# Optimization experiments

Measured on AMD Instinct MI355X. Metric: run time of the kernel, lower is better.

Reference implementation:

```python
import jax, jax.numpy as jnp
import numpy as np

NTOKENS = 6144
SPLIT = 2048          # splits = [0, 2048, inf]
TEMP = 65.0
N, D = 128, 256


def setup_inputs() -> dict:
    key = jax.random.key(0)
    k1, k2, k3, k4, k5, k6 = jax.random.split(key, 6)
    hiddens = jax.random.normal(k1, (N, D), dtype=jnp.float32)
    targets = jax.random.randint(k2, (N,), 0, NTOKENS)
    emb = jax.random.normal(k3, (NTOKENS + 1, D), dtype=jnp.float32)  # +1 tail-target token
    W = jax.random.normal(k4, (D, D), dtype=jnp.float32) / np.sqrt(D)
    U = jax.random.normal(k5, (D, D), dtype=jnp.float32) / np.sqrt(D)
    b = jax.random.normal(k6, (D,), dtype=jnp.float32)
    return {"hiddens": hiddens, "targets": targets, "emb": emb, "W": W, "U": U, "b": b}


def _logprob(h, words_emb, W, U, b):
    # h: [N, d]; words_emb: [V, d]
    # surrogate one-step RNN-cell model: out = tanh(E[w] @ W + h @ U + b) -> [N, V, d]
    out = jnp.tanh(words_emb @ W + (h @ U + b)[:, None, :])
    # SimpleEuclDistance: squared euclidean distance per (hidden, word)
    dist = jnp.sum((h[:, None, :] - out) ** 2, axis=-1)          # [N, V]
    # SimplePolynomialKernel: k(d) = 1 / (1 + d), scaled by temp
    k = TEMP / (1.0 + dist)
    return jax.nn.log_softmax(k, axis=-1)


def reference(hiddens, targets, emb, W, U, b):
    n_head = SPLIT            # head words 0..SPLIT-1
    n_tail = NTOKENS - SPLIT  # tail words SPLIT..NTOKENS-1
    # head vocab = head words + the single tail-target token (index NTOKENS)
    head_ids = jnp.concatenate([jnp.arange(n_head), jnp.array([NTOKENS])])
    lp_head = _logprob(hiddens, emb[head_ids], W, U, b)          # [N, n_head+1]
    lp_tail = _logprob(hiddens, emb[SPLIT:NTOKENS], W, U, b)     # [N, n_tail]

    is_head = targets < SPLIT
    head_idx = jnp.clip(targets, 0, n_head - 1)
    tail_idx = jnp.clip(targets - SPLIT, 0, n_tail - 1)
    head_loss = -jnp.take_along_axis(lp_head, head_idx[:, None], axis=1)[:, 0]
    # for tail tokens: head part is the tail-target column (last col, softmaxed_head_res[:, -1])
    tail_loss = -(lp_head[:, -1] + jnp.take_along_axis(lp_tail, tail_idx[:, None], axis=1)[:, 0])
    per_token = jnp.where(is_head, head_loss, tail_loss)
    return jnp.sum(per_token) / targets.shape[0]
```

## Files before the change

### kernel.cpp

```cpp
#include <hip/hip_runtime.h>
#include <hip/hip_bf16.h>
#include <cfloat>

#define V_ALL  6145
#define SPLIT_ 2048
#define NROW   128
#define DDIM   256
#define TEMP_  65.0f
#define KS     6160

#define EW_OFF 0
#define EW_SZ  (V_ALL * DDIM)
#define HU_OFF (EW_OFF + EW_SZ)
#define HU_SZ  (NROW * DDIM)
#define RL_OFF (HU_OFF + HU_SZ)
#define RL_SZ  NROW
#define K_OFF  ((RL_OFF + RL_SZ + 3) & ~3)

__global__ __launch_bounds__(256) void k_hu(const float* __restrict__ h,
                                            const float* __restrict__ U,
                                            const float* __restrict__ b,
                                            float* __restrict__ hU) {
    const int d = threadIdx.x;
    const int n = blockIdx.x;
    const float4* __restrict__ hr = (const float4*)(h + n * DDIM);
    float acc = b[d];
    #pragma unroll 8
    for (int k4 = 0; k4 < DDIM / 4; ++k4) {
        float4 hv = hr[k4];
        int k = k4 * 4;
        acc = fmaf(hv.x, U[(k + 0) * DDIM + d], acc);
        acc = fmaf(hv.y, U[(k + 1) * DDIM + d], acc);
        acc = fmaf(hv.z, U[(k + 2) * DDIM + d], acc);
        acc = fmaf(hv.w, U[(k + 3) * DDIM + d], acc);
    }
    hU[n * DDIM + d] = acc;
}

__global__ __launch_bounds__(256) void k_ew(const float* __restrict__ emb,
                                            const float* __restrict__ W,
                                            float* __restrict__ EW) {
    const int d = threadIdx.x;
    const int v0 = blockIdx.x * 8;
    const float4* __restrict__ er[8];
    #pragma unroll
    for (int i = 0; i < 8; ++i) {
        int r = v0 + i;
        if (r > V_ALL - 1) r = V_ALL - 1;
        er[i] = (const float4*)(emb + r * DDIM);
    }
    float acc[8];
    #pragma unroll
    for (int i = 0; i < 8; ++i) acc[i] = 0.f;

    for (int k4 = 0; k4 < DDIM / 4; ++k4) {
        const int k = k4 * 4;
        const float w0 = W[(k + 0) * DDIM + d];
        const float w1 = W[(k + 1) * DDIM + d];
        const float w2 = W[(k + 2) * DDIM + d];
        const float w3 = W[(k + 3) * DDIM + d];
        #pragma unroll
        for (int i = 0; i < 8; ++i) {
            float4 e = er[i][k4];
            acc[i] = fmaf(e.x, w0, acc[i]);
            acc[i] = fmaf(e.y, w1, acc[i]);
            acc[i] = fmaf(e.z, w2, acc[i]);
            acc[i] = fmaf(e.w, w3, acc[i]);
        }
    }
    #pragma unroll
    for (int i = 0; i < 8; ++i) {
        int r = v0 + i;
        if (r <= V_ALL - 1) EW[r * DDIM + d] = acc[i];
    }
}

__device__ __forceinline__ float tanh_fast(float x) {
    float ex = __expf(2.f * x);
    return fmaf(-2.f, __builtin_amdgcn_rcpf(ex + 1.f), 1.f);
}

__global__ __launch_bounds__(256) void k_dist(const float* __restrict__ EW,
                                              const float* __restrict__ hU,
                                              const float* __restrict__ h,
                                              float* __restrict__ Km) {
    __shared__ float sEW[16][260];
    __shared__ float sHU[16][260];
    __shared__ float sH [16][260];

    const int v0 = blockIdx.x * 16;
    const int n0 = blockIdx.y * 16;

    #pragma unroll
    for (int j = 0; j < 4; ++j) {
        int idx = threadIdx.x + 256 * j;
        int r   = idx >> 6;
        int c4  = idx & 63;
        int vr  = v0 + r; if (vr > V_ALL - 1) vr = V_ALL - 1;
        *(float4*)&sEW[r][c4 * 4] = *(const float4*)&EW[vr * DDIM + c4 * 4];
        *(float4*)&sHU[r][c4 * 4] = *(const float4*)&hU[(n0 + r) * DDIM + c4 * 4];
        *(float4*)&sH [r][c4 * 4] = *(const float4*)&h [(n0 + r) * DDIM + c4 * 4];
    }
    __syncthreads();

    const int vl = threadIdx.x & 15;
    const int nl = threadIdx.x >> 4;
    const float* pe = &sEW[vl][0];
    const float* pa = &sHU[nl][0];
    const float* ph = &sH [nl][0];

    float acc = 0.f;
    #pragma unroll 4
    for (int d4 = 0; d4 < DDIM / 4; ++d4) {
        float4 e  = *(const float4*)(pe + d4 * 4);
        float4 a  = *(const float4*)(pa + d4 * 4);
        float4 hh = *(const float4*)(ph + d4 * 4);
        { float t = tanh_fast(e.x + a.x); float df = hh.x - t; acc = fmaf(df, df, acc); }
        { float t = tanh_fast(e.y + a.y); float df = hh.y - t; acc = fmaf(df, df, acc); }
        { float t = tanh_fast(e.z + a.z); float df = hh.z - t; acc = fmaf(df, df, acc); }
        { float t = tanh_fast(e.w + a.w); float df = hh.w - t; acc = fmaf(df, df, acc); }
    }
    float kk = TEMP_ / (1.f + acc);
    int vg = v0 + vl;
    if (vg <= V_ALL - 1) Km[(n0 + nl) * KS + vg] = kk;
}

__device__ __forceinline__ float block_max(float x, volatile float* s4) {
    #pragma unroll
    for (int o = 32; o; o >>= 1) x = fmaxf(x, __shfl_down(x, o));
    __syncthreads();
    if ((threadIdx.x & 63) == 0) s4[threadIdx.x >> 6] = x;
    __syncthreads();
    return fmaxf(fmaxf(s4[0], s4[1]), fmaxf(s4[2], s4[3]));
}
__device__ __forceinline__ float block_sum(float x, volatile float* s4) {
    #pragma unroll
    for (int o = 32; o; o >>= 1) x += __shfl_down(x, o);
    __syncthreads();
    if ((threadIdx.x & 63) == 0) s4[threadIdx.x >> 6] = x;
    __syncthreads();
    return s4[0] + s4[1] + s4[2] + s4[3];
}

__global__ __launch_bounds__(256) void k_lse(const float* __restrict__ Km,
                                             const int* __restrict__ targets,
                                             float* __restrict__ rowloss) {
    __shared__ float s4[4];
    const int n = blockIdx.x;
    const int tid = threadIdx.x;
    const float* row = Km + n * KS;

    float m = -FLT_MAX;
    for (int v = tid; v < SPLIT_ + 1; v += 256) {
        int c = (v == SPLIT_) ? (V_ALL - 1) : v;
        m = fmaxf(m, row[c]);
    }
    float hmax = block_max(m, s4);
    float s = 0.f;
    for (int v = tid; v < SPLIT_ + 1; v += 256) {
        int c = (v == SPLIT_) ? (V_ALL - 1) : v;
        s += __expf(row[c] - hmax);
    }
    float hsum = block_sum(s, s4);

    m = -FLT_MAX;
    for (int v = tid; v < 4096; v += 256) m = fmaxf(m, row[SPLIT_ + v]);
    float tmax = block_max(m, s4);
    s = 0.f;
    for (int v = tid; v < 4096; v += 256) s += __expf(row[SPLIT_ + v] - tmax);
    float tsum = block_sum(s, s4);

    if (tid == 0) {
        float logZh = hmax + logf(hsum);
        float logZt = tmax + logf(tsum);
        int t = targets[n];
        float loss;
        if (t < SPLIT_) loss = logZh - row[t];
        else            loss = logZh + logZt - row[V_ALL - 1] - row[t];
        rowloss[n] = loss;
    }
}

__global__ __launch_bounds__(128) void k_final(const float* __restrict__ rowloss,
                                               float* __restrict__ out) {
    const int tid = threadIdx.x;
    float x = rowloss[tid];
    #pragma unroll
    for (int o = 32; o; o >>= 1) x += __shfl_down(x, o);
    __shared__ float s[2];
    if ((tid & 63) == 0) s[tid >> 6] = x;
    __syncthreads();
    if (tid == 0) out[0] = (s[0] + s[1]) / (float)NROW;
}

extern "C" void kernel_launch(void* const* d_in, const int* in_sizes, int n_in,
                              void* d_out, int out_size, void* d_ws, size_t ws_size,
                              hipStream_t stream) {
    const float* h       = (const float*)d_in[0];
    const int*   targets = (const int*)  d_in[1];
    const float* emb     = (const float*)d_in[2];
    const float* W       = (const float*)d_in[3];
    const float* U       = (const float*)d_in[4];
    const float* b       = (const float*)d_in[5];

    float* ws = (float*)d_ws;
    float* EW = ws + EW_OFF;
    float* hU = ws + HU_OFF;
    float* rl = ws + RL_OFF;
    float* Km = ws + K_OFF;

    k_hu  <<<dim3(NROW),      dim3(256), 0, stream>>>(h, U, b, hU);
    k_ew  <<<dim3(769),       dim3(256), 0, stream>>>(emb, W, EW);
    k_dist<<<dim3(385, 8),    dim3(256), 0, stream>>>(EW, hU, h, Km);
    k_lse <<<dim3(NROW),      dim3(256), 0, stream>>>(Km, targets, rl);
    k_final<<<dim3(1),        dim3(128), 0, stream>>>(rl, (float*)d_out);
}
```

Baseline: 188.4 us.

## Fuse softmax sums into distance kernel using fixed max and atomics

The distance kernel now computes exp(k-65) directly, using the known upper bound of k (TEMP), and reduces those values over 16-lane groups. It atomically adds the sums into per-row head and tail accumulators and records the target and tail-token kernel values. This removes the full K matrix write, the separate log-sum-exp kernel and a launch. The tanh scaling by 2/ln2 is folded into the EW and hU precomputation so exp2 can be used directly. In exchange it adds atomic contention and a nondeterministic summation order.

Result: faster. 181.5 us (-3.6%).

```diff
diff --git a/kernel.cpp b/kernel.cpp
--- a/kernel.cpp
+++ b/kernel.cpp
@@ -3,26 +3,32 @@
 #include <cfloat>
 
 #define V_ALL  6145
+#define NTOK   6144
 #define SPLIT_ 2048
 #define NROW   128
 #define DDIM   256
 #define TEMP_  65.0f
-#define KS     6160
+#define C2     2.8853900817779268f
 
 #define EW_OFF 0
 #define EW_SZ  (V_ALL * DDIM)
 #define HU_OFF (EW_OFF + EW_SZ)
 #define HU_SZ  (NROW * DDIM)
-#define RL_OFF (HU_OFF + HU_SZ)
-#define RL_SZ  NROW
-#define K_OFF  ((RL_OFF + RL_SZ + 3) & ~3)
+#define HS_OFF (HU_OFF + HU_SZ)
+#define TS_OFF (HS_OFF + NROW)
+#define KT_OFF (TS_OFF + NROW)
+#define KL_OFF (KT_OFF + NROW)
 
 __global__ __launch_bounds__(256) void k_hu(const float* __restrict__ h,
                                             const float* __restrict__ U,
                                             const float* __restrict__ b,
-                                            float* __restrict__ hU) {
+                                            float* __restrict__ hUs,
+                                            float* __restrict__ hsum,
+                                            float* __restrict__ tsum) {
     const int d = threadIdx.x;
     const int n = blockIdx.x;
+    if (d == 0) hsum[n] = 0.f;
+    if (d == 1) tsum[n] = 0.f;
     const float4* __restrict__ hr = (const float4*)(h + n * DDIM);
     float acc = b[d];
     #pragma unroll 8
@@ -34,12 +40,12 @@
         acc = fmaf(hv.z, U[(k + 2) * DDIM + d], acc);
         acc = fmaf(hv.w, U[(k + 3) * DDIM + d], acc);
     }
-    hU[n * DDIM + d] = acc;
+    hUs[n * DDIM + d] = C2 * acc;
 }
 
 __global__ __launch_bounds__(256) void k_ew(const float* __restrict__ emb,
                                             const float* __restrict__ W,
-                                            float* __restrict__ EW) {
+                                            float* __restrict__ EWs) {
     const int d = threadIdx.x;
     const int v0 = blockIdx.x * 8;
     const float4* __restrict__ er[8];
@@ -71,19 +77,18 @@
     #pragma unroll
     for (int i = 0; i < 8; ++i) {
         int r = v0 + i;
-        if (r <= V_ALL - 1) EW[r * DDIM + d] = acc[i];
-    }
-}
-
-__device__ __forceinline__ float tanh_fast(float x) {
-    float ex = __expf(2.f * x);
-    return fmaf(-2.f, __builtin_amdgcn_rcpf(ex + 1.f), 1.f);
-}
-
-__global__ __launch_bounds__(256) void k_dist(const float* __restrict__ EW,
-                                              const float* __restrict__ hU,
+        if (r <= V_ALL - 1) EWs[r * DDIM + d] = C2 * acc[i];
+    }
+}
+
+__global__ __launch_bounds__(256) void k_dist(const float* __restrict__ EWs,
+                                              const float* __restrict__ hUs,
                                               const float* __restrict__ h,
-                                              float* __restrict__ Km) {
+                                              const int* __restrict__ targets,
+                                              float* __restrict__ hsum,
+                                              float* __restrict__ tsum,
+                                              float* __restrict__ ktarget,
+                                              float* __restrict__ ktail) {
     __shared__ float sEW[16][260];
     __shared__ float sHU[16][260];
     __shared__ float sH [16][260];
@@ -97,9 +102,9 @@
         int r   = idx >> 6;
         int c4  = idx & 63;
         int vr  = v0 + r; if (vr > V_ALL - 1) vr = V_ALL - 1;
-        *(float4*)&sEW[r][c4 * 4] = *(const float4*)&EW[vr * DDIM + c4 * 4];
-        *(float4*)&sHU[r][c4 * 4] = *(const float4*)&hU[(n0 + r) * DDIM + c4 * 4];
-        *(float4*)&sH [r][c4 * 4] = *(const float4*)&h [(n0 + r) * DDIM + c4 * 4];
+        *(float4*)&sEW[r][c4 * 4] = *(const float4*)&EWs[vr * DDIM + c4 * 4];
+        *(float4*)&sHU[r][c4 * 4] = *(const float4*)&hUs[(n0 + r) * DDIM + c4 * 4];
+        *(float4*)&sH [r][c4 * 4] = *(const float4*)&h  [(n0 + r) * DDIM + c4 * 4];
     }
     __syncthreads();
 
@@ -109,88 +114,68 @@
     const float* pa = &sHU[nl][0];
     const float* ph = &sH [nl][0];
 
-    float acc = 0.f;
+    float acc0 = 0.f, acc1 = 0.f;
     #pragma unroll 4
     for (int d4 = 0; d4 < DDIM / 4; ++d4) {
         float4 e  = *(const float4*)(pe + d4 * 4);
         float4 a  = *(const float4*)(pa + d4 * 4);
         float4 hh = *(const float4*)(ph + d4 * 4);
-        { float t = tanh_fast(e.x + a.x); float df = hh.x - t; acc = fmaf(df, df, acc); }
-        { float t = tanh_fast(e.y + a.y); float df = hh.y - t; acc = fmaf(df, df, acc); }
-        { float t = tanh_fast(e.z + a.z); float df = hh.z - t; acc = fmaf(df, df, acc); }
-        { float t = tanh_fast(e.w + a.w); float df = hh.w - t; acc = fmaf(df, df, acc); }
-    }
-    float kk = TEMP_ / (1.f + acc);
-    int vg = v0 + vl;
-    if (vg <= V_ALL - 1) Km[(n0 + nl) * KS + vg] = kk;
-}
-
-__device__ __forceinline__ float block_max(float x, volatile float* s4) {
-    #pragma unroll
-    for (int o = 32; o; o >>= 1) x = fmaxf(x, __shfl_down(x, o));
+        { float ex = __builtin_amdgcn_exp2f(e.x + a.x);
+          float t  = fmaf(-2.f, __builtin_amdgcn_rcpf(ex + 1.f), 1.f);
+          float df = hh.x - t; acc0 = fmaf(df, df, acc0); }
+        { float ex = __builtin_amdgcn_exp2f(e.y + a.y);
+          float t  = fmaf(-2.f, __builtin_amdgcn_rcpf(ex + 1.f), 1.f);
+          float df = hh.y - t; acc1 = fmaf(df, df, acc1); }
+        { float ex = __builtin_amdgcn_exp2f(e.z + a.z);
+          float t  = fmaf(-2.f, __builtin_amdgcn_rcpf(ex + 1.f), 1.f);
+          float df = hh.z - t; acc0 = fmaf(df, df, acc0); }
+        { float ex = __builtin_amdgcn_exp2f(e.w + a.w);
+          float t  = fmaf(-2.f, __builtin_amdgcn_rcpf(ex + 1.f), 1.f);
+          float df = hh.w - t; acc1 = fmaf(df, df, acc1); }
+    }
+    const float kk = TEMP_ / (1.f + acc0 + acc1);
+
+    const int vg = v0 + vl;
+    const int n  = n0 + nl;
+    const bool valid = (vg <= NTOK);
+    float ek = valid ? __expf(kk - 65.f) : 0.f;
+
+    ek += __shfl_xor(ek, 1, 16);
+    ek += __shfl_xor(ek, 2, 16);
+    ek += __shfl_xor(ek, 4, 16);
+    ek += __shfl_xor(ek, 8, 16);
+
+    const bool is_head = (v0 < SPLIT_) || (v0 >= NTOK);
+    if (vl == 0) {
+        float* dst = is_head ? hsum : tsum;
+        atomicAdd(&dst[n], ek);
+    }
+    if (valid) {
+        int tn = targets[n];
+        if (vg == tn)   ktarget[n] = kk;
+        if (vg == NTOK) ktail[n]   = kk;
+    }
+}
+
+__global__ __launch_bounds__(128) void k_loss(const float* __restrict__ hsum,
+                                              const float* __restrict__ tsum,
+                                              const float* __restrict__ ktarget,
+                                              const float* __restrict__ ktail,
+                                              const int* __restrict__ targets,
+                                              float* __restrict__ out) {
+    const int n = threadIdx.x;
+    const float logZh = 65.f + logf(hsum[n]);
+    const int t = targets[n];
+    float loss;
+    if (t < SPLIT_) loss = logZh - ktarget[n];
+    else            loss = logZh + 65.f + logf(tsum[n]) - ktail[n] - ktarget[n];
+
+    #pragma unroll
+    for (int o = 32; o; o >>= 1) loss += __shfl_down(loss, o);
+    __shared__ float s[2];
+    if ((n & 63) == 0) s[n >> 6] = loss;
     __syncthreads();
-    if ((threadIdx.x & 63) == 0) s4[threadIdx.x >> 6] = x;
-    __syncthreads();
-    return fmaxf(fmaxf(s4[0], s4[1]), fmaxf(s4[2], s4[3]));
-}
-__device__ __forceinline__ float block_sum(float x, volatile float* s4) {
-    #pragma unroll
-    for (int o = 32; o; o >>= 1) x += __shfl_down(x, o);
-    __syncthreads();
-    if ((threadIdx.x & 63) == 0) s4[threadIdx.x >> 6] = x;
-    __syncthreads();
-    return s4[0] + s4[1] + s4[2] + s4[3];
-}
-
-__global__ __launch_bounds__(256) void k_lse(const float* __restrict__ Km,
-                                             const int* __restrict__ targets,
-                                             float* __restrict__ rowloss) {
-    __shared__ float s4[4];
-    const int n = blockIdx.x;
-    const int tid = threadIdx.x;
-    const float* row = Km + n * KS;
-
-    float m = -FLT_MAX;
-    for (int v = tid; v < SPLIT_ + 1; v += 256) {
-        int c = (v == SPLIT_) ? (V_ALL - 1) : v;
-        m = fmaxf(m, row[c]);
-    }
-    float hmax = block_max(m, s4);
-    float s = 0.f;
-    for (int v = tid; v < SPLIT_ + 1; v += 256) {
-        int c = (v == SPLIT_) ? (V_ALL - 1) : v;
-        s += __expf(row[c] - hmax);
-    }
-    float hsum = block_sum(s, s4);
-
-    m = -FLT_MAX;
-    for (int v = tid; v < 4096; v += 256) m = fmaxf(m, row[SPLIT_ + v]);
-    float tmax = block_max(m, s4);
-    s = 0.f;
-    for (int v = tid; v < 4096; v += 256) s += __expf(row[SPLIT_ + v] - tmax);
-    float tsum = block_sum(s, s4);
-
-    if (tid == 0) {
-        float logZh = hmax + logf(hsum);
-        float logZt = tmax + logf(tsum);
-        int t = targets[n];
-        float loss;
-        if (t < SPLIT_) loss = logZh - row[t];
-        else            loss = logZh + logZt - row[V_ALL - 1] - row[t];
-        rowloss[n] = loss;
-    }
-}
-
-__global__ __launch_bounds__(128) void k_final(const float* __restrict__ rowloss,
-                                               float* __restrict__ out) {
-    const int tid = threadIdx.x;
-    float x = rowloss[tid];
-    #pragma unroll
-    for (int o = 32; o; o >>= 1) x += __shfl_down(x, o);
-    __shared__ float s[2];
-    if ((tid & 63) == 0) s[tid >> 6] = x;
-    __syncthreads();
-    if (tid == 0) out[0] = (s[0] + s[1]) / (float)NROW;
+    if (n == 0) out[0] = (s[0] + s[1]) / (float)NROW;
 }
 
 extern "C" void kernel_launch(void* const* d_in, const int* in_sizes, int n_in,
@@ -203,15 +188,18 @@
     const float* U       = (const float*)d_in[4];
     const float* b       = (const float*)d_in[5];
 
-    float* ws = (float*)d_ws;
-    float* EW = ws + EW_OFF;
-    float* hU = ws + HU_OFF;
-    float* rl = ws + RL_OFF;
-    float* Km = ws + K_OFF;
-
-    k_hu  <<<dim3(NROW),      dim3(256), 0, stream>>>(h, U, b, hU);
-    k_ew  <<<dim3(769),       dim3(256), 0, stream>>>(emb, W, EW);
-    k_dist<<<dim3(385, 8),    dim3(256), 0, stream>>>(EW, hU, h, Km);
-    k_lse <<<dim3(NROW),      dim3(256), 0, stream>>>(Km, targets, rl);
-    k_final<<<dim3(1),        dim3(128), 0, stream>>>(rl, (float*)d_out);
-}
+    float* ws  = (float*)d_ws;
+    float* EWs = ws + EW_OFF;
+    float* hUs = ws + HU_OFF;
+    float* hs  = ws + HS_OFF;
+    float* ts  = ws + TS_OFF;
+    float* kt  = ws + KT_OFF;
+    float* kl  = ws + KL_OFF;
+
+    k_hu  <<<dim3(NROW),   dim3(256), 0, stream>>>(h, U, b, hUs, hs, ts);
+    k_ew  <<<dim3(769),    dim3(256), 0, stream>>>(emb, W, EWs);
+    k_dist<<<dim3(385, 8), dim3(256), 0, stream>>>(EWs, hUs, h, targets,
+                                                   hs, ts, kt, kl);
+    k_loss<<<dim3(1),      dim3(128), 0, stream>>>(hs, ts, kt, kl, targets,
+                                                   (float*)d_out);
+}
```
